# Kernel optimization log

Hardware: AMD Instinct MI355X
Metric: run time of the kernel (lower is better)

Reference implementation:

```python
import jax, jax.numpy as jnp
import numpy as np

EPS = 1e-8  # torch CosineSimilarity eps


def _neg_indices(N):
    # boolean mask removing diag and the +/-N diagonals, then per-row column
    # indices of the surviving (negative) entries: shape (2N, 2N-2)
    two_n = 2 * N
    mask = ~(np.eye(two_n, dtype=bool)
             | np.eye(two_n, k=N, dtype=bool)
             | np.eye(two_n, k=-N, dtype=bool))
    rows, cols = np.nonzero(mask)  # row-major order matches torch bool indexing
    return cols.reshape(two_n, two_n - 2)


def setup_inputs() -> dict:
    key = jax.random.key(0)
    k1, k2 = jax.random.split(key)
    B, D = 4096, 128
    return {
        "zis": jax.random.normal(k1, (B, D), dtype=jnp.float32),
        "zjs": jax.random.normal(k2, (B, D), dtype=jnp.float32),
    }


def reference(zis, zjs):
    N = zis.shape[0]
    temperature = 0.5
    reps = jnp.concatenate([zjs, zis], axis=0)            # (2N, D)
    norms = jnp.maximum(jnp.linalg.norm(reps, axis=-1, keepdims=True), EPS)
    r = reps / norms
    sim = r @ r.T                                         # (2N, 2N) cosine sims
    l_pos = jnp.diagonal(sim, offset=N)                   # (N,)
    r_pos = jnp.diagonal(sim, offset=-N)                  # (N,)
    positives = jnp.concatenate([l_pos, r_pos])[:, None]  # (2N, 1)
    neg_idx = jnp.asarray(_neg_indices(N))                # (2N, 2N-2) static
    negatives = jnp.take_along_axis(sim, neg_idx, axis=1) # (2N, 2N-2)
    logits = jnp.concatenate([positives, negatives], axis=1) / temperature
    # CrossEntropy with labels all 0, reduction='sum'
    loss = -jnp.sum(jax.nn.log_softmax(logits, axis=-1)[:, 0])
    return loss / (2 * N)
```

## Files before the change

kernel.cpp:

```cpp
#include <hip/hip_runtime.h>
#include <hip/hip_bf16.h>
#include <stdint.h>

typedef __attribute__((ext_vector_type(8))) short bf16x8;
typedef __attribute__((ext_vector_type(4))) float f32x4;

#define TWO_N 8192
#define NHALF 4096
#define DIM   128

#define SQRT_C 1.69864361f
#define LN2    0.69314718055994531f

__device__ __forceinline__ unsigned int f2bf(float f) {
  unsigned int u = __float_as_uint(f);
  u += 0x7FFFu + ((u >> 16) & 1u);
  return u >> 16;
}

__global__ __launch_bounds__(256) void norm_kernel(
    const float* __restrict__ zis, const float* __restrict__ zjs,
    unsigned int* __restrict__ rbf ) {
  const int wave = threadIdx.x >> 6;
  const int lane = threadIdx.x & 63;
  const int row = blockIdx.x * 4 + wave;
  const float* src = (row < NHALF) ? (zjs + (size_t)row * DIM)
                                   : (zis + (size_t)(row - NHALF) * DIM);
  float2 v = ((const float2*)src)[lane];
  float ss = v.x * v.x + v.y * v.y;
#pragma unroll
  for (int m = 1; m <= 32; m <<= 1) ss += __shfl_xor(ss, m);
  const float scale = SQRT_C / fmaxf(sqrtf(ss), 1e-8f);
  const unsigned int lo = f2bf(v.x * scale);
  const unsigned int hi = f2bf(v.y * scale);
  rbf[(size_t)row * (DIM / 2) + lane] = lo | (hi << 16);
}

#define GLL16(SRC, DST) __builtin_amdgcn_global_load_lds( \
    (__attribute__((address_space(1))) void*)(SRC),       \
    (__attribute__((address_space(3))) void*)(DST), 16, 0, 0)

#define STAGE128(ROWBASE, DST) do {                                        \
  _Pragma("unroll")                                                        \
  for (int i_ = 0; i_ < 8; ++i_) {                                         \
    const int L_ = (i_ * 256 + t) * 16;                                    \
    const int row_ = L_ >> 8;                                              \
    const int cb_ = L_ & 255;                                              \
    GLL16(rbytes + (size_t)((ROWBASE) + row_) * 256 +                      \
              (cb_ ^ ((row_ & 7) << 4)),                                   \
          (DST) + L_);                                                     \
  }                                                                        \
} while (0)

__global__ __launch_bounds__(256)
__attribute__((amdgpu_waves_per_eu(2, 2)))
void simloss_kernel(
    const char* __restrict__ rbytes,
    float* __restrict__ pos,
    float* __restrict__ s_part) {
  __shared__ char Bb0[32768];
  __shared__ char Bb1[32768];
  const int t = threadIdx.x;
  const int rb = blockIdx.x >> 3;
  const int cs = blockIdx.x & 7;
  const int RB = rb * 128;
  const int CS = cs * 1024;
  const int wave = t >> 6;
  const int lane = t & 63;
  const int wr = wave >> 1, wc = wave & 1;
  const int lrow = lane >> 4, lcol = lane & 15;

  bf16x8 a_reg[4][4];
#pragma unroll
  for (int ks = 0; ks < 4; ++ks)
#pragma unroll
    for (int m = 0; m < 4; ++m)
      a_reg[ks][m] = *(const bf16x8*)(
          rbytes + (size_t)(RB + wr * 64 + m * 16 + lcol) * 256 +
          ks * 64 + lrow * 16);

  STAGE128(CS, Bb0);
  STAGE128(CS + 128, Bb1);

  float srun[4][4];
#pragma unroll
  for (int m = 0; m < 4; ++m)
#pragma unroll
    for (int r = 0; r < 4; ++r) srun[m][r] = 0.0f;

#pragma unroll 1
  for (int ct = 0; ct < 8; ++ct) {
    if (ct < 7) asm volatile("s_waitcnt vmcnt(8)" ::: "memory");
    else        asm volatile("s_waitcnt vmcnt(0)" ::: "memory");
    __builtin_amdgcn_s_barrier();
    __builtin_amdgcn_sched_barrier(0);

    const char* curB = (ct & 1) ? Bb1 : Bb0;
    bf16x8 bfr[4][4];
#pragma unroll
    for (int n = 0; n < 4; ++n)
#pragma unroll
      for (int ks = 0; ks < 4; ++ks) {
        const int row = wc * 64 + n * 16 + lcol;
        const int kb = ks * 64 + lrow * 16;
        bfr[ks][n] = *(const bf16x8*)(curB + row * 256 + (kb ^ ((row & 7) << 4)));
      }

    f32x4 acc[4][4];
#pragma unroll
    for (int m = 0; m < 4; ++m)
#pragma unroll
      for (int n = 0; n < 4; ++n) acc[m][n] = (f32x4){0.f, 0.f, 0.f, 0.f};

#pragma unroll
    for (int ks = 0; ks < 4; ++ks)
#pragma unroll
      for (int m = 0; m < 4; ++m)
#pragma unroll
        for (int n = 0; n < 4; ++n)
          acc[m][n] = __builtin_amdgcn_mfma_f32_16x16x32_bf16(
              a_reg[ks][m], bfr[ks][n], acc[m][n], 0, 0, 0);

    __builtin_amdgcn_sched_barrier(0);
    __builtin_amdgcn_s_barrier();
    __builtin_amdgcn_sched_barrier(0);
    if (ct < 6) STAGE128(CS + (ct + 2) * 128, (char*)((ct & 1) ? Bb1 : Bb0));

    const int CB = CS + ct * 128;
#pragma unroll
    for (int m = 0; m < 4; ++m) {
      const int R0 = RB + wr * 64 + m * 16;
#pragma unroll
      for (int n = 0; n < 4; ++n) {
        const int C0 = CB + wc * 64 + n * 16;
        const bool hasDiag = (C0 == R0);
        const bool hasPartner = (C0 == (R0 ^ 4096));
#pragma unroll
        for (int r = 0; r < 4; ++r) {
          const float v = acc[m][n][r];
          float e = __builtin_amdgcn_exp2f(v);
          const bool mine = (lcol == lrow * 4 + r);
          if (hasPartner && mine) pos[R0 + lrow * 4 + r] = v;
          if (hasDiag && mine) e = 0.0f;
          srun[m][r] += e;
        }
      }
    }
  }

#pragma unroll
  for (int m = 0; m < 4; ++m)
#pragma unroll
    for (int r = 0; r < 4; ++r) {
      float s = srun[m][r];
      s += __shfl_xor(s, 1);
      s += __shfl_xor(s, 2);
      s += __shfl_xor(s, 4);
      s += __shfl_xor(s, 8);
      if (lcol == 0)
        s_part[(size_t)(cs * 2 + wc) * TWO_N +
               (RB + wr * 64 + m * 16 + lrow * 4 + r)] = s;
    }
}

__global__ __launch_bounds__(256) void reduce1_kernel(
    const float* __restrict__ pos, const float* __restrict__ s_part,
    float* __restrict__ partial) {
  const int t = threadIdx.x;
  const int row = blockIdx.x * 256 + t;
  float s = 0.0f;
#pragma unroll
  for (int q = 0; q < 16; ++q) s += s_part[(size_t)q * TWO_N + row];
  float local = (__log2f(s) - pos[row]) * LN2;
#pragma unroll
  for (int m = 1; m <= 32; m <<= 1) local += __shfl_xor(local, m);
  __shared__ float wsum[4];
  if ((t & 63) == 0) wsum[t >> 6] = local;
  __syncthreads();
  if (t == 0) partial[blockIdx.x] = wsum[0] + wsum[1] + wsum[2] + wsum[3];
}

__global__ __launch_bounds__(64) void reduce2_kernel(
    const float* __restrict__ partial, float* __restrict__ out) {
  float v = (threadIdx.x < 32) ? partial[threadIdx.x] : 0.0f;
#pragma unroll
  for (int m = 1; m <= 32; m <<= 1) v += __shfl_xor(v, m);
  if (threadIdx.x == 0) out[0] = v * (1.0f / TWO_N);
}

extern "C" void kernel_launch(void* const* d_in, const int* in_sizes, int n_in,
                              void* d_out, int out_size, void* d_ws, size_t ws_size,
                              hipStream_t stream) {
  const float* zis = (const float*)d_in[0];
  const float* zjs = (const float*)d_in[1];
  char* ws = (char*)d_ws;
  unsigned int* rbf = (unsigned int*)ws;
  float* pos = (float*)(ws + 2u * 1024 * 1024);
  float* s_part = (float*)(ws + 2u * 1024 * 1024 + 32 * 1024);
  float* partial = (float*)(ws + 2u * 1024 * 1024 + 544 * 1024);

  norm_kernel<<<TWO_N / 4, 256, 0, stream>>>(zis, zjs, rbf);
  simloss_kernel<<<512, 256, 0, stream>>>((const char*)rbf, pos, s_part);
  reduce1_kernel<<<TWO_N / 256, 256, 0, stream>>>(pos, s_part, partial);
  reduce2_kernel<<<1, 64, 0, stream>>>(partial, (float*)d_out);
}
```

Baseline: 86.72 us.

## Split each column tile into four sub-phases interleaving MFMA and exp with barriers

Each 128-column tile is now processed in four 16-column slices. Each slice loads its own B fragments, runs the MFMAs with raised wave priority, then does the exp/accumulate epilogue, so MFMA and transcendental work from different waves can overlap. This also cuts accumulator and B-fragment register use. In exchange it adds a workgroup barrier per slice and moves the next-tile prefetch to after all slices, which may reduce how well loads overlap with compute.

```diff
diff --git a/kernel.cpp b/kernel.cpp
--- a/kernel.cpp
+++ b/kernel.cpp
@@ -88,6 +88,9 @@
 #pragma unroll
     for (int r = 0; r < 4; ++r) srun[m][r] = 0.0f;
 
+  char* curB = Bb0;
+  char* nxtB = Bb1;
+
 #pragma unroll 1
   for (int ct = 0; ct < 8; ++ct) {
     if (ct < 7) asm volatile("s_waitcnt vmcnt(8)" ::: "memory");
@@ -95,49 +98,42 @@
     __builtin_amdgcn_s_barrier();
     __builtin_amdgcn_sched_barrier(0);
 
-    const char* curB = (ct & 1) ? Bb1 : Bb0;
-    bf16x8 bfr[4][4];
-#pragma unroll
-    for (int n = 0; n < 4; ++n)
+    const int CB = CS + ct * 128;
+
+#pragma unroll
+    for (int p = 0; p < 4; ++p) {
+      bf16x8 bfr[4];
 #pragma unroll
       for (int ks = 0; ks < 4; ++ks) {
-        const int row = wc * 64 + n * 16 + lcol;
+        const int row = wc * 64 + p * 16 + lcol;
         const int kb = ks * 64 + lrow * 16;
-        bfr[ks][n] = *(const bf16x8*)(curB + row * 256 + (kb ^ ((row & 7) << 4)));
+        bfr[ks] = *(const bf16x8*)(curB + row * 256 + (kb ^ ((row & 7) << 4)));
       }
-
-    f32x4 acc[4][4];
-#pragma unroll
-    for (int m = 0; m < 4; ++m)
-#pragma unroll
-      for (int n = 0; n < 4; ++n) acc[m][n] = (f32x4){0.f, 0.f, 0.f, 0.f};
-
-#pragma unroll
-    for (int ks = 0; ks < 4; ++ks)
-#pragma unroll
-      for (int m = 0; m < 4; ++m)
-#pragma unroll
-        for (int n = 0; n < 4; ++n)
-          acc[m][n] = __builtin_amdgcn_mfma_f32_16x16x32_bf16(
-              a_reg[ks][m], bfr[ks][n], acc[m][n], 0, 0, 0);
-
-    __builtin_amdgcn_sched_barrier(0);
-    __builtin_amdgcn_s_barrier();
-    __builtin_amdgcn_sched_barrier(0);
-    if (ct < 6) STAGE128(CS + (ct + 2) * 128, (char*)((ct & 1) ? Bb1 : Bb0));
-
-    const int CB = CS + ct * 128;
-#pragma unroll
-    for (int m = 0; m < 4; ++m) {
-      const int R0 = RB + wr * 64 + m * 16;
-#pragma unroll
-      for (int n = 0; n < 4; ++n) {
-        const int C0 = CB + wc * 64 + n * 16;
+      __builtin_amdgcn_s_barrier();
+      __builtin_amdgcn_sched_barrier(0);
+
+      f32x4 acc[4];
+#pragma unroll
+      for (int m = 0; m < 4; ++m) acc[m] = (f32x4){0.f, 0.f, 0.f, 0.f};
+
+      __builtin_amdgcn_s_setprio(1);
+#pragma unroll
+      for (int ks = 0; ks < 4; ++ks)
+#pragma unroll
+        for (int m = 0; m < 4; ++m)
+          acc[m] = __builtin_amdgcn_mfma_f32_16x16x32_bf16(
+              a_reg[ks][m], bfr[ks], acc[m], 0, 0, 0);
+      __builtin_amdgcn_s_setprio(0);
+
+      const int C0 = CB + wc * 64 + p * 16;
+#pragma unroll
+      for (int m = 0; m < 4; ++m) {
+        const int R0 = RB + wr * 64 + m * 16;
         const bool hasDiag = (C0 == R0);
         const bool hasPartner = (C0 == (R0 ^ 4096));
 #pragma unroll
         for (int r = 0; r < 4; ++r) {
-          const float v = acc[m][n][r];
+          const float v = acc[m][r];
           float e = __builtin_amdgcn_exp2f(v);
           const bool mine = (lcol == lrow * 4 + r);
           if (hasPartner && mine) pos[R0 + lrow * 4 + r] = v;
@@ -146,6 +142,12 @@
         }
       }
     }
+
+    __builtin_amdgcn_s_barrier();
+    __builtin_amdgcn_sched_barrier(0);
+    if (ct < 6) STAGE128(CS + (ct + 2) * 128, curB);
+
+    char* tmp = curB; curB = nxtB; nxtB = tmp;
   }
 
 #pragma unroll
```

After: 87.54 us. About the same (+0.9%).
